# Performance work log

Measured on AMD Instinct MI355X. Metric: run time of the kernel, lower is better.

The kernel has to match this reference:

```python
import jax, jax.numpy as jnp
from jax import lax
import numpy as np

N_STEPS = 6  # fixed-grid dopri5 steps over t in [0,1] (stands in for adaptive solve at rtol=atol=1e-3)
EPS = 1e-5


def group_norm(x, w, b, groups=32):
    B, C, H, W = x.shape
    xr = x.reshape(B, groups, -1)
    m = xr.mean(-1, keepdims=True)
    v = xr.var(-1, keepdims=True)
    xn = ((xr - m) * lax.rsqrt(v + EPS)).reshape(B, C, H, W)
    return xn * w[None, :, None, None] + b[None, :, None, None]


def conv2d(x, w, b, stride, pad):
    y = lax.conv_general_dilated(x, w, (stride, stride), [(pad, pad), (pad, pad)],
                                 dimension_numbers=('NCHW', 'OIHW', 'NCHW'))
    return y + b[None, :, None, None]


def make_odefunc(oa_w, oa_b, occ1_w, occ1_b, ob_w, ob_b, occ2_w, occ2_b, oc_w, oc_b):
    def f(t, x):
        B, _, H, W = x.shape
        tt = jnp.full((B, 1, H, W), t, x.dtype)
        h = jax.nn.relu(group_norm(x, oa_w, oa_b))
        h = conv2d(jnp.concatenate([tt, h], axis=1), occ1_w, occ1_b, 1, 1)
        h = jax.nn.relu(group_norm(h, ob_w, ob_b))
        h = conv2d(jnp.concatenate([tt, h], axis=1), occ2_w, occ2_b, 1, 1)
        return group_norm(h, oc_w, oc_b)
    return f


def dopri5_fixed(f, y0, t0=0.0, t1=1.0, n=N_STEPS):
    h = (t1 - t0) / n
    def step(y, i):
        t = t0 + i * h
        k1 = f(t, y)
        k2 = f(t + h * (1/5),  y + h * (1/5) * k1)
        k3 = f(t + h * (3/10), y + h * ((3/40) * k1 + (9/40) * k2))
        k4 = f(t + h * (4/5),  y + h * ((44/45) * k1 + (-56/15) * k2 + (32/9) * k3))
        k5 = f(t + h * (8/9),  y + h * ((19372/6561) * k1 + (-25360/2187) * k2 + (64448/6561) * k3 + (-212/729) * k4))
        k6 = f(t + h,          y + h * ((9017/3168) * k1 + (-355/33) * k2 + (46732/5247) * k3 + (49/176) * k4 + (-5103/18656) * k5))
        y1 = y + h * ((35/384) * k1 + (500/1113) * k3 + (125/192) * k4 + (-2187/6784) * k5 + (11/84) * k6)
        return y1, None
    y, _ = lax.scan(step, y0, jnp.arange(n, dtype=jnp.float32))
    return y


def setup_inputs() -> dict:
    key = jax.random.key(0)
    ks = jax.random.split(key, 8)
    d = {}
    d['x'] = jax.random.normal(ks[0], (256, 3, 32, 32), jnp.float32)
    d['c1_w'] = jax.random.normal(ks[1], (64, 3, 3, 3), jnp.float32) * 0.1
    d['c1_b'] = jnp.zeros((64,), jnp.float32)
    d['g1_w'] = jnp.ones((64,), jnp.float32); d['g1_b'] = jnp.zeros((64,), jnp.float32)
    d['c2_w'] = jax.random.normal(ks[2], (64, 64, 4, 4), jnp.float32) * 0.05
    d['c2_b'] = jnp.zeros((64,), jnp.float32)
    d['g2_w'] = jnp.ones((64,), jnp.float32); d['g2_b'] = jnp.zeros((64,), jnp.float32)
    d['c3_w'] = jax.random.normal(ks[3], (64, 64, 4, 4), jnp.float32) * 0.05
    d['c3_b'] = jnp.zeros((64,), jnp.float32)
    d['oa_w'] = jnp.ones((64,), jnp.float32); d['oa_b'] = jnp.zeros((64,), jnp.float32)
    d['occ1_w'] = jax.random.normal(ks[4], (64, 65, 3, 3), jnp.float32) * 0.05
    d['occ1_b'] = jnp.zeros((64,), jnp.float32)
    d['ob_w'] = jnp.ones((64,), jnp.float32); d['ob_b'] = jnp.zeros((64,), jnp.float32)
    d['occ2_w'] = jax.random.normal(ks[5], (64, 65, 3, 3), jnp.float32) * 0.05
    d['occ2_b'] = jnp.zeros((64,), jnp.float32)
    d['oc_w'] = jnp.ones((64,), jnp.float32); d['oc_b'] = jnp.zeros((64,), jnp.float32)
    d['g3_w'] = jnp.ones((64,), jnp.float32); d['g3_b'] = jnp.zeros((64,), jnp.float32)
    d['lin_w'] = jax.random.normal(ks[6], (10, 64), jnp.float32) * 0.1
    d['lin_b'] = jnp.zeros((10,), jnp.float32)
    return d


def reference(x, c1_w, c1_b, g1_w, g1_b, c2_w, c2_b, g2_w, g2_b, c3_w, c3_b,
              oa_w, oa_b, occ1_w, occ1_b, ob_w, ob_b, occ2_w, occ2_b, oc_w, oc_b,
              g3_w, g3_b, lin_w, lin_b):
    h = jax.nn.relu(group_norm(conv2d(x, c1_w, c1_b, 1, 0), g1_w, g1_b))   # [B,64,30,30]
    h = jax.nn.relu(group_norm(conv2d(h, c2_w, c2_b, 2, 1), g2_w, g2_b))   # [B,64,15,15]
    h = conv2d(h, c3_w, c3_b, 2, 1)                                        # [B,64,7,7]
    f = make_odefunc(oa_w, oa_b, occ1_w, occ1_b, ob_w, ob_b, occ2_w, occ2_b, oc_w, oc_b)
    h = dopri5_fixed(f, h)                                                 # ODE solve t:0->1
    h = jax.nn.relu(group_norm(h, g3_w, g3_b))
    h = h.mean(axis=(2, 3))                                                # adaptive avg pool (1,1) + flatten
    return h @ lin_w.T + lin_b                                             # [B,10]
```

## Files before the change

kernel.cpp:

```cpp
#include <hip/hip_runtime.h>
#include <hip/hip_bf16.h>

#define B 256
#define NELEM 3136
#define TOTAL (B*NELEM)

typedef __attribute__((ext_vector_type(8))) short bf16x8;
typedef __attribute__((ext_vector_type(4))) float f32x4;

#define MFMA16(a,b,c) __builtin_amdgcn_mfma_f32_16x16x32_bf16((a),(b),(c),0,0,0)

__device__ __forceinline__ unsigned short f2bf(float f) {
    unsigned u = __float_as_uint(f);
    unsigned r = (u + 0x7fffu + ((u >> 16) & 1u)) >> 16;
    return (unsigned short)r;
}
__device__ __forceinline__ unsigned int f2bf2(float lo, float hi) {
    return (unsigned int)f2bf(lo) | ((unsigned int)f2bf(hi) << 16);
}

__device__ const int d_sigma[64] = {
    6,12,13,19,0,20,1,7,2,8,3,9,4,10,5,11,
    18,24,25,31,26,32,27,33,14,34,15,21,16,22,17,23,
    30,36,37,43,38,44,39,45,40,46,41,47,28,48,29,35,
    42,42,42,42,42,42,42,42,42,42,42,42,42,42,42,42
};

__global__ __launch_bounds__(256) void prep_afrag_kernel(
    const float* __restrict__ w1, const float* __restrict__ w2,
    short* __restrict__ af1, short* __restrict__ af2)
{
    const int e = blockIdx.x * 256 + threadIdx.x;
    const float* W = blockIdx.y ? w2 : w1;
    short* dst = blockIdx.y ? af2 : af1;
    const int j = e & 7;
    const int lane = (e >> 3) & 63;
    const int kt = (e >> 9) % 18;
    const int mt = (e >> 9) / 18;
    const int m = mt*16 + (lane & 15);
    const int k = kt*32 + ((lane >> 4) & 3)*8 + j;
    const int tap = k >> 6;
    const int ic  = k & 63;
    dst[e] = (short)f2bf(W[m*585 + (ic + 1)*9 + tap]);
}

__global__ __launch_bounds__(256) void prep_stab_kernel(
    const float* __restrict__ w1, const float* __restrict__ w2,
    float* __restrict__ stab1, float* __restrict__ stab2)
{
    const int id = blockIdx.x * 256 + threadIdx.x;
    if (id >= 3136) return;
    const float* W = blockIdx.y ? w2 : w1;
    float* dst = blockIdx.y ? stab2 : stab1;
    const int oc = id / 49, p = id % 49;
    const int py = p / 7, px = p % 7;
    float s = 0.f;
    #pragma unroll
    for (int ky = 0; ky < 3; ++ky) {
        int iy = py - 1 + ky;
        if (iy < 0 || iy > 6) continue;
        #pragma unroll
        for (int kx = 0; kx < 3; ++kx) {
            int ix = px - 1 + kx;
            if (ix < 0 || ix > 6) continue;
            s += W[oc*585 + ky*3 + kx];
        }
    }
    dst[id] = s;
}

__global__ __launch_bounds__(256) void prep_c1frag_kernel(
    const float* __restrict__ w1, short* __restrict__ afc1)
{
    const int e = blockIdx.x * 256 + threadIdx.x;
    const int j = e & 7, lane = (e >> 3) & 63, mtq = e >> 9;
    const int m = mtq*16 + (lane & 15);
    const int k = ((lane >> 4) & 3)*8 + j;
    float v = (k < 27) ? w1[m*27 + k] : 0.f;
    afc1[e] = (short)f2bf(v);
}

__global__ __launch_bounds__(256) void prep_c23frag_kernel(
    const float* __restrict__ w2, const float* __restrict__ w3,
    short* __restrict__ afc2, short* __restrict__ afc3)
{
    const int e = blockIdx.x * 256 + threadIdx.x;
    const float* W = blockIdx.y ? w3 : w2;
    short* dst = blockIdx.y ? afc3 : afc2;
    const int j = e & 7, lane = (e >> 3) & 63, kt = (e >> 9) & 31, mtq = e >> 14;
    const int m = mtq*16 + (lane & 15);
    const int k = kt*32 + ((lane >> 4) & 3)*8 + j;
    const int tap = k >> 6, ic = k & 63;
    dst[e] = (short)f2bf(W[m*1024 + ic*16 + tap]);
}

__global__ __launch_bounds__(512, 1) void conv1_fused(
    const float* __restrict__ x, const short* __restrict__ afc1,
    const float* __restrict__ bias,
    const float* __restrict__ g1w, const float* __restrict__ g1b,
    short* __restrict__ h1pad)
{
    __shared__ float xs[3072];
    __shared__ float gnred[128], gnq[128];
    __shared__ float s_mean[32], s_rstd[32];

    const int t = threadIdx.x, b = blockIdx.x;
    const int w = t >> 6, l = t & 63, lhi = (l >> 4) & 3, llo = l & 15;
    const int mt = w & 3, sub = w >> 2;
    const int oc0 = mt*16 + lhi*4;

    for (int i = t; i < 3072; i += 512) xs[i] = x[b*3072 + i];

    bf16x8 afr = *(const bf16x8*)(afc1 + ((size_t)(mt*64 + l))*8);

    int boff[8]; bool bval[8];
    #pragma unroll
    for (int j = 0; j < 8; ++j) {
        int k = lhi*8 + j;
        bval[j] = (k < 27);
        int kk = bval[j] ? k : 0;
        int c = kk / 9, tap = kk % 9;
        boff[j] = c*1024 + (tap/3)*32 + (tap%3);
    }
    f32x4 bia = *(const f32x4*)&bias[oc0];
    __syncthreads();

    f32x4 acc[29];
    float s[4] = {0,0,0,0}, q[4] = {0,0,0,0};
    #pragma unroll
    for (int i = 0; i < 29; ++i) {
        const int nt = sub*29 + i;
        f32x4 a = {0.f,0.f,0.f,0.f};
        if (nt < 57) {
            const int p = nt*16 + llo;
            const int pc = p < 900 ? p : 899;
            const int base = (pc/30)*32 + (pc%30);
            union { bf16x8 v; unsigned u[4]; } bb;
            #pragma unroll
            for (int jj = 0; jj < 4; ++jj) {
                float e0 = bval[2*jj]   ? xs[boff[2*jj]   + base] : 0.f;
                float e1 = bval[2*jj+1] ? xs[boff[2*jj+1] + base] : 0.f;
                bb.u[jj] = f2bf2(e0, e1);
            }
            a = MFMA16(afr, bb.v, a);
            #pragma unroll
            for (int r = 0; r < 4; ++r) {
                a[r] += bia[r];
                if (p < 900) { s[r] += a[r]; q[r] += a[r]*a[r]; }
            }
        }
        acc[i] = a;
// ... 161 lines not shown
    const float b0 = g2b[oc0], b1v_ = g2b[oc0+1], b2v_ = g2b[oc0+2], b3v_ = g2b[oc0+3];
    char* hb2 = (char*)h2pad + (size_t)b*36992;

    #pragma unroll
    for (int i = 0; i < 8; ++i) {
        const int nt = half*8 + i;
        if (nt > 14) continue;
        const int n = nt*16 + llo;
        if (n >= 225) continue;
        const int pidx = (n/15 + 1)*17 + (n%15 + 1);
        float v0 = fmaxf((acc[i][0]-m0)*rs0*w0  + b0,   0.f);
        float v1 = fmaxf((acc[i][1]-m0)*rs0*w1v + b1v_, 0.f);
        float v2 = fmaxf((acc[i][2]-m1)*rs1*w2v + b2v_, 0.f);
        float v3 = fmaxf((acc[i][3]-m1)*rs1*w3v + b3v_, 0.f);
        uint2 pk; pk.x = f2bf2(v0, v1); pk.y = f2bf2(v2, v3);
        *(uint2*)(hb2 + (oc0>>3)*4624 + pidx*16 + ((oc0&7)<<1)) = pk;
    }
    if (t < 512) {
        const int bp = t >> 3, c8 = t & 7;
        int pidx;
        if (bp < 17) pidx = bp;
        else if (bp < 34) pidx = 16*17 + (bp - 17);
        else if (bp < 49) pidx = (bp - 34 + 1)*17;
        else pidx = (bp - 49 + 1)*17 + 16;
        uint4 z; z.x = z.y = z.z = z.w = 0u;
        *(uint4*)(hb2 + c8*4624 + pidx*16) = z;
    }
}

__global__ __launch_bounds__(512, 1) void conv3_mfma(
    const short* __restrict__ h2pad, const short* __restrict__ afc3,
    const float* __restrict__ bias, float* __restrict__ y)
{
    __shared__ __align__(16) char sin[36992];
    const int t = threadIdx.x, b = blockIdx.x;
    const int w = t >> 6, l = t & 63, lhi = (l >> 4) & 3, llo = l & 15;
    const int mt = w >> 1, half = w & 1;
    const int oc0 = mt*16 + lhi*4;

    {
        const uint4* src = (const uint4*)((const char*)h2pad + (size_t)b*36992);
        uint4* dst = (uint4*)sin;
        for (int i = t; i < 2312; i += 512) dst[i] = src[i];
    }
    bf16x8 aw[32];
    #pragma unroll
    for (int kt = 0; kt < 32; ++kt)
        aw[kt] = *(const bf16x8*)(afc3 + ((size_t)((mt*32 + kt)*64 + l))*8);
    f32x4 bia = *(const f32x4*)&bias[oc0];
    __syncthreads();

    f32x4 acc[2];
    acc[0] = (f32x4){0.f,0.f,0.f,0.f};
    acc[1] = (f32x4){0.f,0.f,0.f,0.f};
    #pragma unroll
    for (int i = 0; i < 2; ++i) {
        const int nt = half*2 + i;
        const int n = nt*16 + llo;
        const int p = n < 49 ? n : 48;
        const int oy = p/7, ox = p%7;
        #pragma unroll
        for (int kt = 0; kt < 32; ++kt) {
            const int tap = kt >> 1;
            const int ky = tap >> 2, kx = tap & 3;
            const int pidx = (oy*2 + ky)*17 + (ox*2 + kx);
            const int c8 = (kt & 1)*4 + lhi;
            bf16x8 bb = *(const bf16x8*)(sin + c8*4624 + pidx*16);
            acc[i] = MFMA16(aw[kt], bb, acc[i]);
        }
    }
    #pragma unroll
    for (int i = 0; i < 2; ++i) {
        const int n = (half*2 + i)*16 + llo;
        if (n < 49) {
            #pragma unroll
            for (int r = 0; r < 4; ++r)
                y[(size_t)b*NELEM + (oc0 + r)*49 + n] = acc[i][r] + bia[r];
        }
    }
}

#define SGRP 104
#define KSTR 3328
#define ODE_LDS 115456
__global__ __launch_bounds__(512, 1) void ode_head(
    const float* __restrict__ yin,
    const short* __restrict__ af1, const short* __restrict__ af2,
    const float* __restrict__ stab1, const float* __restrict__ stab2,
    const float* __restrict__ b1v, const float* __restrict__ b2v,
    const float* __restrict__ oaw, const float* __restrict__ oab,
    const float* __restrict__ obw, const float* __restrict__ obb,
    const float* __restrict__ ocw, const float* __restrict__ ocb,
    const float* __restrict__ g3w, const float* __restrict__ g3b,
    const float* __restrict__ linw, const float* __restrict__ linb,
    float* __restrict__ out)
{
    extern __shared__ char smem[];
    float* y_l    = (float*)smem;
    float* kbuf   = (float*)(smem + 13312);
    char*  act0   = smem + 93184;
    char*  act1   = smem + 103552;
    float* gnred  = (float*)(smem + 113920);
    float* soaw   = (float*)(smem + 114432);
    float* soab   = (float*)(smem + 114688);
    float* s_mean = (float*)(smem + 114944);
    float* s_rstd = (float*)(smem + 115072);
    float* s_cm   = (float*)(smem + 115200);

    const int t = threadIdx.x, b = blockIdx.x;
    const int w = t >> 6, l = t & 63, lhi = (l >> 4) & 3, llo = l & 15;
    const int mt = w >> 1;
    const int ntA = (w & 1)*2, ntB = ntA + 1;
    const int nA = ntA*16 + llo, nB = ntB*16 + llo;
    const bool vA = nA < 49, vB = nB < 49;
    const int pxA = d_sigma[nA], pxB = d_sigma[nB];
    const int paA = (pxA/7 + 1)*9 + (pxA%7 + 1);
    const int paB = (pxB/7 + 1)*9 + (pxB%7 + 1);
    const int oc0 = mt*16 + lhi*4;
    const int g16 = t >> 4, sub = t & 15;

    for (int u = t; u < 3136; u += 512) {
        const int g = u / 98, e = u - g*98;
        y_l[g*SGRP + e] = yin[(size_t)b*NELEM + u];
    }
    for (int i = t; i < 5184; i += 512) ((unsigned*)act0)[i] = 0u;
    if (t < 64) { soaw[t] = oaw[t]; soab[t] = oab[t]; }

    float stabA1[4], stabB1[4], stabA2[4], stabB2[4];
    #pragma unroll
    for (int r = 0; r < 4; ++r) {
        stabA1[r] = stab1[(oc0 + r)*49 + pxA];
        stabB1[r] = stab1[(oc0 + r)*49 + pxB];
        stabA2[r] = stab2[(oc0 + r)*49 + pxA];
        stabB2[r] = stab2[(oc0 + r)*49 + pxB];
    }
    const f32x4 bia1 = *(const f32x4*)&b1v[oc0];
    const f32x4 bia2 = *(const f32x4*)&b2v[oc0];
    const f32x4 gwB = *(const f32x4*)&obw[oc0];
    const f32x4 gbB = *(const f32x4*)&obb[oc0];
    const f32x4 gwC = *(const f32x4*)&ocw[oc0];
    const f32x4 gbC = *(const f32x4*)&ocb[oc0];
    __syncthreads();

    const float hf  = (float)(1.0/6.0);
    const float C10 = (float)((1.0/6.0)*(1.0/5.0));
    const float C20 = (float)((1.0/6.0)*(3.0/40.0)),  C21 = (float)((1.0/6.0)*(9.0/40.0));
    const float C30 = (float)((1.0/6.0)*(44.0/45.0)), C31 = (float)((1.0/6.0)*(-56.0/15.0)), C32 = (float)((1.0/6.0)*(32.0/9.0));
    const float C40 = (float)((1.0/6.0)*(19372.0/6561.0)), C41 = (float)((1.0/6.0)*(-25360.0/2187.0)),
                C42 = (float)((1.0/6.0)*(64448.0/6561.0)), C43 = (float)((1.0/6.0)*(-212.0/729.0));
    const float C50 = (float)((1.0/6.0)*(9017.0/3168.0)), C51 = (float)((1.0/6.0)*(-355.0/33.0)),
                C52 = (float)((1.0/6.0)*(46732.0/5247.0)), C53 = (float)((1.0/6.0)*(49.0/176.0)),
                C54 = (float)((1.0/6.0)*(-5103.0/18656.0));
    const float B0 = (float)((1.0/6.0)*(35.0/384.0)), B2c = (float)((1.0/6.0)*(500.0/1113.0)),
                B3c = (float)((1.0/6.0)*(125.0/192.0)), B4c = (float)((1.0/6.0)*(-2187.0/6784.0)),
                B5c = (float)((1.0/6.0)*(11.0/84.0));

    for (int step = 0; step < 6; ++step) {
        const float t0 = (float)step * hf;
        for (int stage = 0; stage < 6; ++stage) {
            float cA=0.f, cB=0.f, cC=0.f, cD=0.f, cE=0.f, tf=0.f;
            if (stage == 1)      { cA=C10; tf = 0.2f; }
            else if (stage == 2) { cA=C20; cB=C21; tf = 0.3f; }
            else if (stage == 3) { cA=C30; cB=C31; cC=C32; tf = 0.8f; }
            else if (stage == 4) { cA=C40; cB=C41; cC=C42; cD=C43; tf = (float)(8.0/9.0); }
            else if (stage == 5) { cA=C50; cB=C51; cC=C52; cD=C53; cE=C54; tf = 1.f; }
            const float tval = t0 + hf*tf;

            {
                const float* Yg = y_l + g16*SGRP;
                const float* Kg = kbuf + g16*SGRP;
                const int e0 = 4*sub;
                const int n1 = (sub < 8) ? 4 : ((sub == 8) ? 2 : 0);
                const int e1 = 64 + 4*sub;

                f32x4 va, vb = {0.f,0.f,0.f,0.f};
                {
                    f32x4 xv = *(const f32x4*)(Yg + e0);
                    if (stage > 0) xv += cA * *(const f32x4*)(Kg + 0*KSTR + e0);
                    if (stage > 1) xv += cB * *(const f32x4*)(Kg + 1*KSTR + e0);
                    if (stage > 2) xv += cC * *(const f32x4*)(Kg + 2*KSTR + e0);
                    if (stage > 3) xv += cD * *(const f32x4*)(Kg + 3*KSTR + e0);
                    if (stage > 4) xv += cE * *(const f32x4*)(Kg + 4*KSTR + e0);
                    va = xv;
                }
                if (n1 == 4) {
                    f32x4 xv = *(const f32x4*)(Yg + e1);
                    if (stage > 0) xv += cA * *(const f32x4*)(Kg + 0*KSTR + e1);
                    if (stage > 1) xv += cB * *(const f32x4*)(Kg + 1*KSTR + e1);
                    if (stage > 2) xv += cC * *(const f32x4*)(Kg + 2*KSTR + e1);
                    if (stage > 3) xv += cD * *(const f32x4*)(Kg + 3*KSTR + e1);
                    if (stage > 4) xv += cE * *(const f32x4*)(Kg + 4*KSTR + e1);
                    vb = xv;
                } else if (n1 == 2) {
                    float x0 = Yg[96], x1 = Yg[97];
                    if (stage > 0) { x0 = fmaf(cA, Kg[0*KSTR+96], x0); x1 = fmaf(cA, Kg[0*KSTR+97], x1); }
                    if (stage > 1) { x0 = fmaf(cB, Kg[1*KSTR+96], x0); x1 = fmaf(cB, Kg[1*KSTR+97], x1); }
                    if (stage > 2) { x0 = fmaf(cC, Kg[2*KSTR+96], x0); x1 = fmaf(cC, Kg[2*KSTR+97], x1); }
                    if (stage > 3) { x0 = fmaf(cD, Kg[3*KSTR+96], x0); x1 = fmaf(cD, Kg[3*KSTR+97], x1); }
                    if (stage > 4) { x0 = fmaf(cE, Kg[4*KSTR+96], x0); x1 = fmaf(cE, Kg[4*KSTR+97], x1); }
                    vb[0] = x0; vb[1] = x1;
                }

                float s = va[0]+va[1]+va[2]+va[3];
                float q = va[0]*va[0]+va[1]*va[1]+va[2]*va[2]+va[3]*va[3];
                if (n1 >= 2) { s += vb[0]+vb[1]; q += vb[0]*vb[0]+vb[1]*vb[1]; }
                if (n1 == 4) { s += vb[2]+vb[3]; q += vb[2]*vb[2]+vb[3]*vb[3]; }
                s += __shfl_xor(s, 1); q += __shfl_xor(q, 1);
                s += __shfl_xor(s, 2); q += __shfl_xor(q, 2);
                s += __shfl_xor(s, 4); q += __shfl_xor(q, 4);
                s += __shfl_xor(s, 8); q += __shfl_xor(q, 8);
                const float m = s * (1.f/98.f);
                const float rs = rsqrtf(q * (1.f/98.f) - m*m + 1e-5f);
                const float w0 = soaw[2*g16], w1s = soaw[2*g16+1];
                const float bb0 = soab[2*g16], bb1 = soab[2*g16+1];

                #pragma unroll
                for (int j2 = 0; j2 < 4; ++j2) {
                    const int e = e0 + j2;
                    const int odd = e >= 49 ? 1 : 0;
                    const int ch = 2*g16 + odd;
                    const int p = e - 49*odd;
                    float nv = fmaxf((va[j2] - m)*rs*(odd ? w1s : w0) + (odd ? bb1 : bb0), 0.f);
                    const int pa = (p/7 + 1)*9 + (p%7) + 1;
                    *(unsigned short*)(act0 + (ch>>3)*1296 + pa*16 + ((ch&7)<<1)) = f2bf(nv);
                }
                for (int j2 = 0; j2 < n1; ++j2) {
                    const int e = e1 + j2;
                    const int odd = e >= 49 ? 1 : 0;
                    const int ch = 2*g16 + odd;
                    const int p = e - 49*odd;
                    float nv = fmaxf((vb[j2] - m)*rs*(odd ? w1s : w0) + (odd ? bb1 : bb0), 0.f);
                    const int pa = (p/7 + 1)*9 + (p%7) + 1;
                    *(unsigned short*)(act0 + (ch>>3)*1296 + pa*16 + ((ch&7)<<1)) = f2bf(nv);
                }
            }
            __syncthreads();

            float v0[4], v1[4];
            {
                bf16x8 aw[18];
                #pragma unroll
                for (int kt = 0; kt < 18; ++kt)
                    aw[kt] = *(const bf16x8*)(af1 + ((size_t)(mt*18 + kt)*64 + l)*8);
                f32x4 acc0 = {0.f,0.f,0.f,0.f}, acc1 = {0.f,0.f,0.f,0.f};
                #pragma unroll
                for (int kt = 0; kt < 18; ++kt) {
                    const int tap = kt >> 1;
                    const int dB = ((tap/3 - 1)*9 + (tap%3 - 1))*16;
                    const int cb = ((kt & 1)*4 + lhi)*1296;
                    bf16x8 bb0 = *(const bf16x8*)(act0 + cb + paA*16 + dB);
                    bf16x8 bb1 = *(const bf16x8*)(act0 + cb + paB*16 + dB);
                    acc0 = MFMA16(aw[kt], bb0, acc0);
                    acc1 = MFMA16(aw[kt], bb1, acc1);
                }
                #pragma unroll
                for (int r = 0; r < 4; ++r) {
                    v0[r] = acc0[r] + bia1[r] + tval * stabA1[r];
                    v1[r] = acc1[r] + bia1[r] + tval * stabB1[r];
                }
            }
            {
                float s0=0.f,q0=0.f,s1=0.f,q1=0.f;
                if (vA) { s0 += v0[0]+v0[1]; q0 += v0[0]*v0[0]+v0[1]*v0[1];
                          s1 += v0[2]+v0[3]; q1 += v0[2]*v0[2]+v0[3]*v0[3]; }
                if (vB) { s0 += v1[0]+v1[1]; q0 += v1[0]*v1[0]+v1[1]*v1[1];
                          s1 += v1[2]+v1[3]; q1 += v1[2]*v1[2]+v1[3]*v1[3]; }
                #pragma unroll
                for (int off = 1; off < 16; off <<= 1) {
                    s0 += __shfl_xor(s0, off); q0 += __shfl_xor(q0, off);
                    s1 += __shfl_xor(s1, off); q1 += __shfl_xor(q1, off);
                }
                if (llo == 0) {
                    float* gp = gnred + w*16 + lhi*4;
                    gp[0]=s0; gp[1]=q0; gp[2]=s1; gp[3]=q1;
                }
            }
            __syncthreads();
            {
                const int gb = mt*32 + lhi*4;
                const float sg0 = gnred[gb]   + gnred[gb+16];
                const float qg0 = gnred[gb+1] + gnred[gb+17];
                const float sg1 = gnred[gb+2] + gnred[gb+18];
                const float qg1 = gnred[gb+3] + gnred[gb+19];
                const float m0 = sg0*(1.f/98.f);
                const float r0 = rsqrtf(qg0*(1.f/98.f) - m0*m0 + 1e-5f);
                const float m1 = sg1*(1.f/98.f);
                const float r1 = rsqrtf(qg1*(1.f/98.f) - m1*m1 + 1e-5f);
                v0[0] = fmaxf((v0[0]-m0)*r0*gwB[0]+gbB[0], 0.f);
                v0[1] = fmaxf((v0[1]-m0)*r0*gwB[1]+gbB[1], 0.f);
                v0[2] = fmaxf((v0[2]-m1)*r1*gwB[2]+gbB[2], 0.f);
                v0[3] = fmaxf((v0[3]-m1)*r1*gwB[3]+gbB[3], 0.f);
                v1[0] = fmaxf((v1[0]-m0)*r0*gwB[0]+gbB[0], 0.f);
                v1[1] = fmaxf((v1[1]-m0)*r0*gwB[1]+gbB[1], 0.f);
                v1[2] = fmaxf((v1[2]-m1)*r1*gwB[2]+gbB[2], 0.f);
                v1[3] = fmaxf((v1[3]-m1)*r1*gwB[3]+gbB[3], 0.f);
                if (vA) {
                    uint2 pk; pk.x = f2bf2(v0[0], v0[1]); pk.y = f2bf2(v0[2], v0[3]);
                    *(uint2*)(act1 + (oc0>>3)*1296 + paA*16 + ((oc0&7)<<1)) = pk;
                }
                if (vB) {
                    uint2 pk; pk.x = f2bf2(v1[0], v1[1]); pk.y = f2bf2(v1[2], v1[3]);
                    *(uint2*)(act1 + (oc0>>3)*1296 + paB*16 + ((oc0&7)<<1)) = pk;
                }
            }
            __syncthreads();

            {
                bf16x8 aw[18];
                #pragma unroll
                for (int kt = 0; kt < 18; ++kt)
                    aw[kt] = *(const bf16x8*)(af2 + ((size_t)(mt*18 + kt)*64 + l)*8);
                f32x4 acc0 = {0.f,0.f,0.f,0.f}, acc1 = {0.f,0.f,0.f,0.f};
                #pragma unroll
                for (int kt = 0; kt < 18; ++kt) {
                    const int tap = kt >> 1;
                    const int dB = ((tap/3 - 1)*9 + (tap%3 - 1))*16;
                    const int cb = ((kt & 1)*4 + lhi)*1296;
                    bf16x8 bb0 = *(const bf16x8*)(act1 + cb + paA*16 + dB);
                    bf16x8 bb1 = *(const bf16x8*)(act1 + cb + paB*16 + dB);
                    acc0 = MFMA16(aw[kt], bb0, acc0);
                    acc1 = MFMA16(aw[kt], bb1, acc1);
                }
                #pragma unroll
                for (int r = 0; r < 4; ++r) {
                    v0[r] = acc0[r] + bia2[r] + tval * stabA2[r];
                    v1[r] = acc1[r] + bia2[r] + tval * stabB2[r];
                }
            }
            {
                float s0=0.f,q0=0.f,s1=0.f,q1=0.f;
                if (vA) { s0 += v0[0]+v0[1]; q0 += v0[0]*v0[0]+v0[1]*v0[1];
                          s1 += v0[2]+v0[3]; q1 += v0[2]*v0[2]+v0[3]*v0[3]; }
                if (vB) { s0 += v1[0]+v1[1]; q0 += v1[0]*v1[0]+v1[1]*v1[1];
                          s1 += v1[2]+v1[3]; q1 += v1[2]*v1[2]+v1[3]*v1[3]; }
                #pragma unroll
                for (int off = 1; off < 16; off <<= 1) {
                    s0 += __shfl_xor(s0, off); q0 += __shfl_xor(q0, off);
                    s1 += __shfl_xor(s1, off); q1 += __shfl_xor(q1, off);
                }
                if (llo == 0) {
                    float* gp = gnred + w*16 + lhi*4;
                    gp[0]=s0; gp[1]=q0; gp[2]=s1; gp[3]=q1;
                }
            }
            __syncthreads();
            {
                const int gb = mt*32 + lhi*4;
                const float sg0 = gnred[gb]   + gnred[gb+16];
                const float qg0 = gnred[gb+1] + gnred[gb+17];
                const float sg1 = gnred[gb+2] + gnred[gb+18];
                const float qg1 = gnred[gb+3] + gnred[gb+19];
                const float m0 = sg0*(1.f/98.f);
                const float r0 = rsqrtf(qg0*(1.f/98.f) - m0*m0 + 1e-5f);
                const float m1 = sg1*(1.f/98.f);
                const float r1 = rsqrtf(qg1*(1.f/98.f) - m1*m1 + 1e-5f);
                float* kd = kbuf + stage*KSTR;
                const int gA = oc0 >> 1;
                if (vA) {
                    kd[gA*SGRP + pxA]            = (v0[0]-m0)*r0*gwC[0]+gbC[0];
                    kd[gA*SGRP + 49 + pxA]       = (v0[1]-m0)*r0*gwC[1]+gbC[1];
                    kd[(gA+1)*SGRP + pxA]        = (v0[2]-m1)*r1*gwC[2]+gbC[2];
                    kd[(gA+1)*SGRP + 49 + pxA]   = (v0[3]-m1)*r1*gwC[3]+gbC[3];
                }
                if (vB) {
                    kd[gA*SGRP + pxB]            = (v1[0]-m0)*r0*gwC[0]+gbC[0];
                    kd[gA*SGRP + 49 + pxB]       = (v1[1]-m0)*r0*gwC[1]+gbC[1];
                    kd[(gA+1)*SGRP + pxB]        = (v1[2]-m1)*r1*gwC[2]+gbC[2];
                    kd[(gA+1)*SGRP + 49 + pxB]   = (v1[3]-m1)*r1*gwC[3]+gbC[3];
                }
            }
            __syncthreads();

            if (stage == 5) {
                float* Yg = y_l + g16*SGRP;
                const float* Kg = kbuf + g16*SGRP;
                const int e0 = 4*sub;
                {
                    f32x4 v = *(const f32x4*)(Yg + e0);
                    v += B0  * *(const f32x4*)(Kg + 0*KSTR + e0);
                    v += B2c * *(const f32x4*)(Kg + 2*KSTR + e0);
                    v += B3c * *(const f32x4*)(Kg + 3*KSTR + e0);
                    v += B4c * *(const f32x4*)(Kg + 4*KSTR + e0);
                    v += B5c * *(const f32x4*)(Kg + 5*KSTR + e0);
                    *(f32x4*)(Yg + e0) = v;
                }
                if (sub < 8) {
                    const int e1 = 64 + 4*sub;
                    f32x4 v = *(const f32x4*)(Yg + e1);
                    v += B0  * *(const f32x4*)(Kg + 0*KSTR + e1);
                    v += B2c * *(const f32x4*)(Kg + 2*KSTR + e1);
                    v += B3c * *(const f32x4*)(Kg + 3*KSTR + e1);
                    v += B4c * *(const f32x4*)(Kg + 4*KSTR + e1);
                    v += B5c * *(const f32x4*)(Kg + 5*KSTR + e1);
                    *(f32x4*)(Yg + e1) = v;
                } else if (sub == 8) {
                    #pragma unroll
                    for (int j2 = 0; j2 < 2; ++j2) {
                        const int e = 96 + j2;
                        float v = Yg[e];
                        v = fmaf(B0,  Kg[0*KSTR+e], v);
                        v = fmaf(B2c, Kg[2*KSTR+e], v);
                        v = fmaf(B3c, Kg[3*KSTR+e], v);
                        v = fmaf(B4c, Kg[4*KSTR+e], v);
                        v = fmaf(B5c, Kg[5*KSTR+e], v);
                        Yg[e] = v;
                    }
                }
                __syncthreads();
            }
        }
    }

    {
        float s = 0.f, q = 0.f;
        const float* Yg = y_l + g16*SGRP;
        for (int e = sub; e < 98; e += 16) {
            float v = Yg[e];
            s += v; q += v*v;
        }
        s += __shfl_xor(s,1); q += __shfl_xor(q,1);
        s += __shfl_xor(s,2); q += __shfl_xor(q,2);
        s += __shfl_xor(s,4); q += __shfl_xor(q,4);
        s += __shfl_xor(s,8); q += __shfl_xor(q,8);
        if (sub == 0) {
            float m = s * (1.f/98.f);
            float var = q * (1.f/98.f) - m*m;
            s_mean[g16] = m; s_rstd[g16] = rsqrtf(var + 1e-5f);
        }
    }
    __syncthreads();
    if (t < 64) {
        const int ch = t, g = ch >> 1;
        const float m = s_mean[g], r = s_rstd[g];
        const float ww = g3w[ch], bb = g3b[ch];
        const float* Yc = y_l + g*SGRP + (ch & 1)*49;
        float sum = 0.f;
        for (int p = 0; p < 49; ++p) {
            float v = (Yc[p] - m)*r*ww + bb;
            sum += fmaxf(v, 0.f);
        }
        s_cm[ch] = sum * (1.f/49.f);
    }
    __syncthreads();
    if (t < 10) {
        float a = linb[t];
        for (int c = 0; c < 64; ++c) a = fmaf(s_cm[c], linw[t*64 + c], a);
        out[b*10 + t] = a;
    }
}

extern "C" void kernel_launch(void* const* d_in, const int* in_sizes, int n_in,
                              void* d_out, int out_size, void* d_ws, size_t ws_size,
                              hipStream_t stream)
{
    const float* x      = (const float*)d_in[0];
    const float* c1_w   = (const float*)d_in[1];
    const float* c1_b   = (const float*)d_in[2];
    const float* g1_w   = (const float*)d_in[3];
    const float* g1_b   = (const float*)d_in[4];
    const float* c2_w   = (const float*)d_in[5];
    const float* c2_b   = (const float*)d_in[6];
    const float* g2_w   = (const float*)d_in[7];
    const float* g2_b   = (const float*)d_in[8];
    const float* c3_w   = (const float*)d_in[9];
    const float* c3_b   = (const float*)d_in[10];
    const float* oa_w   = (const float*)d_in[11];
    const float* oa_b   = (const float*)d_in[12];
    const float* occ1_w = (const float*)d_in[13];
    const float* occ1_b = (const float*)d_in[14];
    const float* ob_w   = (const float*)d_in[15];
    const float* ob_b   = (const float*)d_in[16];
    const float* occ2_w = (const float*)d_in[17];
    const float* occ2_b = (const float*)d_in[18];
    const float* oc_w   = (const float*)d_in[19];
    const float* oc_b   = (const float*)d_in[20];
    const float* g3_w   = (const float*)d_in[21];
    const float* g3_b   = (const float*)d_in[22];
    const float* lin_w  = (const float*)d_in[23];
    const float* lin_b  = (const float*)d_in[24];
    float* out = (float*)d_out;

    float* ws = (float*)d_ws;
    size_t off = 0;
    float* y     = ws + off; off += 802816;
    float* stab1 = ws + off; off += 3136;
    float* stab2 = ws + off; off += 3136;
    short* af1   = (short*)(ws + off); off += 18432;
    short* af2   = (short*)(ws + off); off += 18432;
    short* afc1  = (short*)(ws + off); off += 1024;
    short* afc2  = (short*)(ws + off); off += 32768;
    short* afc3  = (short*)(ws + off); off += 32768;
    short* h1pad = (short*)(ws + off); off += 8396800;
    short* h2pad = (short*)(ws + off); off += 2367488;

    prep_afrag_kernel<<<dim3(144, 2), 256, 0, stream>>>(occ1_w, occ2_w, af1, af2);
    prep_stab_kernel<<<dim3(13, 2), 256, 0, stream>>>(occ1_w, occ2_w, stab1, stab2);
    prep_c1frag_kernel<<<8, 256, 0, stream>>>(c1_w, afc1);
    prep_c23frag_kernel<<<dim3(256, 2), 256, 0, stream>>>(c2_w, c3_w, afc2, afc3);

    conv1_fused<<<B, 512, 0, stream>>>(x, afc1, c1_b, g1_w, g1_b, h1pad);
    conv2_fused<<<B, 512, CONV2_LDS, stream>>>(h1pad, afc2, c2_b, g2_w, g2_b, h2pad);
    conv3_mfma<<<B, 512, 0, stream>>>(h2pad, afc3, c3_b, y);

    ode_head<<<B, 512, ODE_LDS, stream>>>(y, af1, af2, stab1, stab2,
        occ1_b, occ2_b, oa_w, oa_b, ob_w, ob_b, oc_w, oc_b,
        g3_w, g3_b, lin_w, lin_b, out);
}
```

Baseline: 251.7 us.

## Switch ODE convs to 32x32 MFMA with register-resident weights and wave specialization

Replaces the 16x16x32 MFMA ODE convolutions with 32x32x16 MFMA. The time channel is folded into two extra K channels in the activation buffer, which removes the precomputed t*stab correction. Weight fragments for both convs are preloaded once into registers, with waves 0-1 running conv1 and waves 2-3 running conv2. Group-norm reductions now happen within a wave via shuffles instead of through LDS, removing one barrier per conv. The cost is that only 2 of 8 waves do MFMA work in each phase, and the kernel carries heavy register pressure from holding 37 bf16x8 fragments plus 32 accumulators.

Measured after the change: 453.6 us. 1.8x slower.

```diff
diff --git a/kernel.cpp b/kernel.cpp
--- a/kernel.cpp
+++ b/kernel.cpp
@@ -5,10 +5,12 @@
 #define NELEM 3136
 #define TOTAL (B*NELEM)
 
-typedef __attribute__((ext_vector_type(8))) short bf16x8;
-typedef __attribute__((ext_vector_type(4))) float f32x4;
+typedef __attribute__((ext_vector_type(8)))  short bf16x8;
+typedef __attribute__((ext_vector_type(4)))  float f32x4;
+typedef __attribute__((ext_vector_type(16))) float f32x16;
 
 #define MFMA16(a,b,c) __builtin_amdgcn_mfma_f32_16x16x32_bf16((a),(b),(c),0,0,0)
+#define MFMA32(a,b,c) __builtin_amdgcn_mfma_f32_32x32x16_bf16((a),(b),(c),0,0,0)
 
 __device__ __forceinline__ unsigned short f2bf(float f) {
     unsigned u = __float_as_uint(f);
@@ -18,55 +20,40 @@
 __device__ __forceinline__ unsigned int f2bf2(float lo, float hi) {
     return (unsigned int)f2bf(lo) | ((unsigned int)f2bf(hi) << 16);
 }
-
-__device__ const int d_sigma[64] = {
-    6,12,13,19,0,20,1,7,2,8,3,9,4,10,5,11,
-    18,24,25,31,26,32,27,33,14,34,15,21,16,22,17,23,
-    30,36,37,43,38,44,39,45,40,46,41,47,28,48,29,35,
-    42,42,42,42,42,42,42,42,42,42,42,42,42,42,42,42
+__device__ __forceinline__ unsigned int cvtpk(float lo, float hi) {
+    unsigned int r;
+    asm("v_cvt_pk_bf16_f32 %0, %1, %2" : "=v"(r) : "v"(lo), "v"(hi));
+    return r;
+}
+
+__device__ const int d_sig32[64] = {
+     6,13, 0, 1, 2, 3, 4, 5,  12,19,20, 7, 8, 9,10,11,
+    18,25,26,27,14,15,16,17,  24,31,32,33,34,21,22,23,
+    30,37,38,39,40,41,28,29,  36,43,44,45,46,47,48,35,
+    42,13, 0, 1, 2, 3, 4, 5,   6,13, 0, 1, 2, 3, 4, 5
 };
 
-__global__ __launch_bounds__(256) void prep_afrag_kernel(
+__global__ __launch_bounds__(256) void prep_af32(
     const float* __restrict__ w1, const float* __restrict__ w2,
-    short* __restrict__ af1, short* __restrict__ af2)
+    short* __restrict__ af1x, short* __restrict__ af2x)
 {
     const int e = blockIdx.x * 256 + threadIdx.x;
+    if (e >= 37888) return;
     const float* W = blockIdx.y ? w2 : w1;
-    short* dst = blockIdx.y ? af2 : af1;
-    const int j = e & 7;
-    const int lane = (e >> 3) & 63;
-    const int kt = (e >> 9) % 18;
-    const int mt = (e >> 9) / 18;
-    const int m = mt*16 + (lane & 15);
-    const int k = kt*32 + ((lane >> 4) & 3)*8 + j;
-    const int tap = k >> 6;
-    const int ic  = k & 63;
-    dst[e] = (short)f2bf(W[m*585 + (ic + 1)*9 + tap]);
-}
-
-__global__ __launch_bounds__(256) void prep_stab_kernel(
-    const float* __restrict__ w1, const float* __restrict__ w2,
-    float* __restrict__ stab1, float* __restrict__ stab2)
-{
-    const int id = blockIdx.x * 256 + threadIdx.x;
-    if (id >= 3136) return;
-    const float* W = blockIdx.y ? w2 : w1;
-    float* dst = blockIdx.y ? stab2 : stab1;
-    const int oc = id / 49, p = id % 49;
-    const int py = p / 7, px = p % 7;
-    float s = 0.f;
-    #pragma unroll
-    for (int ky = 0; ky < 3; ++ky) {
-        int iy = py - 1 + ky;
-        if (iy < 0 || iy > 6) continue;
-        #pragma unroll
-        for (int kx = 0; kx < 3; ++kx) {
-            int ix = px - 1 + kx;
-            if (ix < 0 || ix > 6) continue;
-            s += W[oc*585 + ky*3 + kx];
-        }
-    }
-    dst[id] = s;
+    short* dst = blockIdx.y ? af2x : af1x;
+    const int j = e & 7, lane = (e >> 3) & 63, r = e >> 9;
+    const int kt = r % 37, mh = r / 37;
+    const int m = mh*32 + (lane & 31);
+    const int kk = (lane >> 5)*8 + j;
+    float val;
+    if (kt < 36) {
+        const int tap = kt >> 2;
+        const int ic  = (kt & 3)*16 + kk;
+        val = W[m*585 + (ic + 1)*9 + tap];
+    } else {
+        val = (kk < 9) ? W[m*585 + kk] : 0.f;
+    }
+    dst[e] = (short)f2bf(val);
 }
 
 __global__ __launch_bounds__(256) void prep_c1frag_kernel(
@@ -394,11 +381,19 @@
 
 #define SGRP 104
 #define KSTR 3328
-#define ODE_LDS 115456
-__global__ __launch_bounds__(512, 1) void ode_head(
+#define ACT_C8 1296
+#define ODE_LDS 121408
+#define P_B1 0
+#define P_B2 64
+#define P_GWB 128
+#define P_GBB 192
+#define P_GWC 256
+#define P_GBC 320
+#define P_OAW 384
+#define P_OAB 448
+__global__ __launch_bounds__(512, 2) void ode_head(
     const float* __restrict__ yin,
-    const short* __restrict__ af1, const short* __restrict__ af2,
-    const float* __restrict__ stab1, const float* __restrict__ stab2,
+    const short* __restrict__ af1x, const short* __restrict__ af2x,
     const float* __restrict__ b1v, const float* __restrict__ b2v,
     const float* __restrict__ oaw, const float* __restrict__ oab,
     const float* __restrict__ obw, const float* __restrict__ obb,
@@ -408,50 +403,41 @@
     float* __restrict__ out)
 {
     extern __shared__ char smem[];
-    float* y_l    = (float*)smem;
-    float* kbuf   = (float*)(smem + 13312);
-    char*  act0   = smem + 93184;
-    char*  act1   = smem + 103552;
-    float* gnred  = (float*)(smem + 113920);
-    float* soaw   = (float*)(smem + 114432);
-    float* soab   = (float*)(smem + 114688);
-    float* s_mean = (float*)(smem + 114944);
-    float* s_rstd = (float*)(smem + 115072);
-    float* s_cm   = (float*)(smem + 115200);
+    float* y_l  = (float*)smem;
+    float* kbuf = (float*)(smem + 13312);
+    char*  act0 = smem + 93184;
+    char*  act1 = smem + 106144;
+    float* prm  = (float*)(smem + 119104);
+    float* s_cm = (float*)(smem + 121152);
 
     const int t = threadIdx.x, b = blockIdx.x;
-    const int w = t >> 6, l = t & 63, lhi = (l >> 4) & 3, llo = l & 15;
-    const int mt = w >> 1;
-    const int ntA = (w & 1)*2, ntB = ntA + 1;
-    const int nA = ntA*16 + llo, nB = ntB*16 + llo;
-    const bool vA = nA < 49, vB = nB < 49;
-    const int pxA = d_sigma[nA], pxB = d_sigma[nB];
-    const int paA = (pxA/7 + 1)*9 + (pxA%7 + 1);
-    const int paB = (pxB/7 + 1)*9 + (pxB%7 + 1);
-    const int oc0 = mt*16 + lhi*4;
+    const int w = t >> 6, l = t & 63;
     const int g16 = t >> 4, sub = t & 15;
+
+    const int hi_ = l >> 5;
+    const int ln  = l & 31;
+    const int px0 = d_sig32[ln], px1 = d_sig32[32 + ln];
+    const bool val1 = (32 + ln) <= 48;
+    const int pa0 = (px0/7 + 1)*9 + (px0%7 + 1);
+    const int pa1 = (px1/7 + 1)*9 + (px1%7 + 1);
+    const int mh = w & 1;
 
     for (int u = t; u < 3136; u += 512) {
         const int g = u / 98, e = u - g*98;
         y_l[g*SGRP + e] = yin[(size_t)b*NELEM + u];
     }
-    for (int i = t; i < 5184; i += 512) ((unsigned*)act0)[i] = 0u;
-    if (t < 64) { soaw[t] = oaw[t]; soab[t] = oab[t]; }
-
-    float stabA1[4], stabB1[4], stabA2[4], stabB2[4];
-    #pragma unroll
-    for (int r = 0; r < 4; ++r) {
-        stabA1[r] = stab1[(oc0 + r)*49 + pxA];
-        stabB1[r] = stab1[(oc0 + r)*49 + pxB];
-        stabA2[r] = stab2[(oc0 + r)*49 + pxA];
-        stabB2[r] = stab2[(oc0 + r)*49 + pxB];
-    }
-    const f32x4 bia1 = *(const f32x4*)&b1v[oc0];
-    const f32x4 bia2 = *(const f32x4*)&b2v[oc0];
-    const f32x4 gwB = *(const f32x4*)&obw[oc0];
-    const f32x4 gbB = *(const f32x4*)&obb[oc0];
-    const f32x4 gwC = *(const f32x4*)&ocw[oc0];
-    const f32x4 gbC = *(const f32x4*)&ocb[oc0];
+    for (int i = t; i < 6480; i += 512) ((unsigned*)act0)[i] = 0u;
+    if (t < 64) {
+        prm[P_B1  + t] = b1v[t]; prm[P_B2  + t] = b2v[t];
+        prm[P_GWB + t] = obw[t]; prm[P_GBB + t] = obb[t];
+        prm[P_GWC + t] = ocw[t]; prm[P_GBC + t] = ocb[t];
+        prm[P_OAW + t] = oaw[t]; prm[P_OAB + t] = oab[t];
+    }
+    const short* aft = (w < 2) ? af1x : af2x;
+    bf16x8 afr[37];
+    #pragma unroll
+    for (int kt = 0; kt < 37; ++kt)
+        afr[kt] = *(const bf16x8*)(aft + ((size_t)(mh*37 + kt)*64 + l)*8);
     __syncthreads();
 
     const float hf  = (float)(1.0/6.0);
@@ -523,8 +509,8 @@
                 s += __shfl_xor(s, 8); q += __shfl_xor(q, 8);
                 const float m = s * (1.f/98.f);
                 const float rs = rsqrtf(q * (1.f/98.f) - m*m + 1e-5f);
-                const float w0 = soaw[2*g16], w1s = soaw[2*g16+1];
-                const float bb0 = soab[2*g16], bb1 = soab[2*g16+1];
+                const float w0 = prm[P_OAW + 2*g16], w1c = prm[P_OAW + 2*g16 + 1];
+                const float c0 = prm[P_OAB + 2*g16], c1c = prm[P_OAB + 2*g16 + 1];
 
                 #pragma unroll
                 for (int j2 = 0; j2 < 4; ++j2) {
@@ -532,153 +518,184 @@
                     const int odd = e >= 49 ? 1 : 0;
                     const int ch = 2*g16 + odd;
                     const int p = e - 49*odd;
-                    float nv = fmaxf((va[j2] - m)*rs*(odd ? w1s : w0) + (odd ? bb1 : bb0), 0.f);
+                    float nv = fmaxf((va[j2] - m)*rs*(odd ? w1c : w0) + (odd ? c1c : c0), 0.f);
                     const int pa = (p/7 + 1)*9 + (p%7) + 1;
-                    *(unsigned short*)(act0 + (ch>>3)*1296 + pa*16 + ((ch&7)<<1)) = f2bf(nv);
+                    *(unsigned short*)(act0 + (ch>>3)*ACT_C8 + pa*16 + ((ch&7)<<1)) = f2bf(nv);
                 }
                 for (int j2 = 0; j2 < n1; ++j2) {
                     const int e = e1 + j2;
                     const int odd = e >= 49 ? 1 : 0;
                     const int ch = 2*g16 + odd;
                     const int p = e - 49*odd;
-                    float nv = fmaxf((vb[j2] - m)*rs*(odd ? w1s : w0) + (odd ? bb1 : bb0), 0.f);
+                    float nv = fmaxf((vb[j2] - m)*rs*(odd ? w1c : w0) + (odd ? c1c : c0), 0.f);
                     const int pa = (p/7 + 1)*9 + (p%7) + 1;
-                    *(unsigned short*)(act0 + (ch>>3)*1296 + pa*16 + ((ch&7)<<1)) = f2bf(nv);
-                }
+                    *(unsigned short*)(act0 + (ch>>3)*ACT_C8 + pa*16 + ((ch&7)<<1)) = f2bf(nv);
+                }
+            }
+            if (w == 7 && l < 49) {
+                const int py = l / 7, pxx = l % 7;
+                const int pa = (py + 1)*9 + (pxx + 1);
+                const unsigned tb = (unsigned)f2bf(tval);
+                unsigned h[8];
+                #pragma unroll
+                for (int tap = 0; tap < 8; ++tap) {
+                    const int dy = tap/3 - 1, dx = tap%3 - 1;
+                    const bool ok = ((unsigned)(py+dy) < 7u) && ((unsigned)(pxx+dx) < 7u);
+                    h[tap] = ok ? tb : 0u;
+                }
+                uint4 blkA;
+                blkA.x = h[0] | (h[1]<<16); blkA.y = h[2] | (h[3]<<16);
+                blkA.z = h[4] | (h[5]<<16); blkA.w = h[6] | (h[7]<<16);
+                const bool ok8 = (py+1) < 7 && (pxx+1) < 7;
+                uint4 blkB; blkB.x = ok8 ? tb : 0u; blkB.y = 0u; blkB.z = 0u; blkB.w = 0u;
+                *(uint4*)(act0 + 8*ACT_C8 + pa*16) = blkA;
+                *(uint4*)(act0 + 9*ACT_C8 + pa*16) = blkB;
+                *(uint4*)(act1 + 8*ACT_C8 + pa*16) = blkA;
+                *(uint4*)(act1 + 9*ACT_C8 + pa*16) = blkB;
             }
             __syncthreads();
 
-            float v0[4], v1[4];
-            {
-                bf16x8 aw[18];
-                #pragma unroll
-                for (int kt = 0; kt < 18; ++kt)
-                    aw[kt] = *(const bf16x8*)(af1 + ((size_t)(mt*18 + kt)*64 + l)*8);
-                f32x4 acc0 = {0.f,0.f,0.f,0.f}, acc1 = {0.f,0.f,0.f,0.f};
-                #pragma unroll
-                for (int kt = 0; kt < 18; ++kt) {
-                    const int tap = kt >> 1;
-                    const int dB = ((tap/3 - 1)*9 + (tap%3 - 1))*16;
-                    const int cb = ((kt & 1)*4 + lhi)*1296;
-                    bf16x8 bb0 = *(const bf16x8*)(act0 + cb + paA*16 + dB);
-                    bf16x8 bb1 = *(const bf16x8*)(act0 + cb + paB*16 + dB);
-                    acc0 = MFMA16(aw[kt], bb0, acc0);
-                    acc1 = MFMA16(aw[kt], bb1, acc1);
-                }
-                #pragma unroll
-                for (int r = 0; r < 4; ++r) {
-                    v0[r] = acc0[r] + bia1[r] + tval * stabA1[r];
-                    v1[r] = acc1[r] + bia1[r] + tval * stabB1[r];
-                }
-            }
-            {
-                float s0=0.f,q0=0.f,s1=0.f,q1=0.f;
-                if (vA) { s0 += v0[0]+v0[1]; q0 += v0[0]*v0[0]+v0[1]*v0[1];
-                          s1 += v0[2]+v0[3]; q1 += v0[2]*v0[2]+v0[3]*v0[3]; }
-                if (vB) { s0 += v1[0]+v1[1]; q0 += v1[0]*v1[0]+v1[1]*v1[1];
-                          s1 += v1[2]+v1[3]; q1 += v1[2]*v1[2]+v1[3]*v1[3]; }
-                #pragma unroll
-                for (int off = 1; off < 16; off <<= 1) {
-                    s0 += __shfl_xor(s0, off); q0 += __shfl_xor(q0, off);
-                    s1 += __shfl_xor(s1, off); q1 += __shfl_xor(q1, off);
-                }
-                if (llo == 0) {
-                    float* gp = gnred + w*16 + lhi*4;
-                    gp[0]=s0; gp[1]=q0; gp[2]=s1; gp[3]=q1;
+            if (w < 2) {
+                f32x16 a0, a1;
+                #pragma unroll
+                for (int i = 0; i < 16; ++i) { a0[i] = 0.f; a1[i] = 0.f; }
+                #pragma unroll
+                for (int kt = 0; kt < 37; ++kt) {
+                    int cb, dB;
+                    if (kt < 36) {
+                        const int tap = kt >> 2;
+                        dB = ((tap/3 - 1)*9 + (tap%3 - 1))*16;
+                        cb = ((kt & 3)*2 + hi_)*ACT_C8;
+                    } else { dB = 0; cb = (8 + hi_)*ACT_C8; }
+                    bf16x8 b0 = *(const bf16x8*)(act0 + cb + pa0*16 + dB);
+                    bf16x8 b1 = *(const bf16x8*)(act0 + cb + pa1*16 + dB);
+                    a0 = MFMA32(afr[kt], b0, a0);
+                    a1 = MFMA32(afr[kt], b1, a1);
+                }
+                #pragma unroll
+                for (int qd = 0; qd < 4; ++qd) {
+                    f32x4 bia = *(const f32x4*)&prm[P_B1 + mh*32 + qd*8 + 4*hi_];
+                    #pragma unroll
+                    for (int j = 0; j < 4; ++j) { a0[qd*4+j] += bia[j]; a1[qd*4+j] += bia[j]; }
+                }
+                float gm[8], gr[8];
+                {
+                    float gs[8], gq[8];
+                    #pragma unroll
+                    for (int qd = 0; qd < 4; ++qd)
+                        #pragma unroll
+                        for (int u = 0; u < 2; ++u) {
+                            const int i0 = qd*4 + 2*u;
+                            float s = a0[i0] + a0[i0+1];
+                            float qq = a0[i0]*a0[i0] + a0[i0+1]*a0[i0+1];
+                            if (val1) { s += a1[i0] + a1[i0+1]; qq += a1[i0]*a1[i0] + a1[i0+1]*a1[i0+1]; }
+                            gs[qd*2+u] = s; gq[qd*2+u] = qq;
+                        }
+                    #pragma unroll
+                    for (int off = 1; off < 32; off <<= 1)
+                        #pragma unroll
+                        for (int i = 0; i < 8; ++i) {
+                            gs[i] += __shfl_xor(gs[i], off);
+                            gq[i] += __shfl_xor(gq[i], off);
+                        }
+                    #pragma unroll
+                    for (int i = 0; i < 8; ++i) {
+                        const float m = gs[i]*(1.f/98.f);
+                        gm[i] = m; gr[i] = rsqrtf(gq[i]*(1.f/98.f) - m*m + 1e-5f);
+                    }
+                }
+                #pragma unroll
+                for (int qd = 0; qd < 4; ++qd) {
+                    f32x4 gw = *(const f32x4*)&prm[P_GWB + mh*32 + qd*8 + 4*hi_];
+                    f32x4 gc = *(const f32x4*)&prm[P_GBB + mh*32 + qd*8 + 4*hi_];
+                    const int c8 = mh*4 + qd;
+                    float x0[4], x1[4];
+                    #pragma unroll
+                    for (int u = 0; u < 2; ++u) {
+                        const float m = gm[qd*2+u], r = gr[qd*2+u];
+                        #pragma unroll
+                        for (int j = 0; j < 2; ++j) {
+                            const int i = qd*4 + 2*u + j;
+                            x0[2*u+j] = fmaxf((a0[i]-m)*r*gw[2*u+j] + gc[2*u+j], 0.f);
+                            x1[2*u+j] = fmaxf((a1[i]-m)*r*gw[2*u+j] + gc[2*u+j], 0.f);
+                        }
+                    }
+                    uint2 p0; p0.x = cvtpk(x0[0], x0[1]); p0.y = cvtpk(x0[2], x0[3]);
+                    *(uint2*)(act1 + c8*ACT_C8 + pa0*16 + hi_*8) = p0;
+                    if (val1) {
+                        uint2 p1; p1.x = cvtpk(x1[0], x1[1]); p1.y = cvtpk(x1[2], x1[3]);
+                        *(uint2*)(act1 + c8*ACT_C8 + pa1*16 + hi_*8) = p1;
+                    }
                 }
             }
             __syncthreads();
-            {
-                const int gb = mt*32 + lhi*4;
-                const float sg0 = gnred[gb]   + gnred[gb+16];
-                const float qg0 = gnred[gb+1] + gnred[gb+17];
-                const float sg1 = gnred[gb+2] + gnred[gb+18];
-                const float qg1 = gnred[gb+3] + gnred[gb+19];
-                const float m0 = sg0*(1.f/98.f);
-                const float r0 = rsqrtf(qg0*(1.f/98.f) - m0*m0 + 1e-5f);
-                const float m1 = sg1*(1.f/98.f);
-                const float r1 = rsqrtf(qg1*(1.f/98.f) - m1*m1 + 1e-5f);
-                v0[0] = fmaxf((v0[0]-m0)*r0*gwB[0]+gbB[0], 0.f);
-                v0[1] = fmaxf((v0[1]-m0)*r0*gwB[1]+gbB[1], 0.f);
-                v0[2] = fmaxf((v0[2]-m1)*r1*gwB[2]+gbB[2], 0.f);
-                v0[3] = fmaxf((v0[3]-m1)*r1*gwB[3]+gbB[3], 0.f);
-                v1[0] = fmaxf((v1[0]-m0)*r0*gwB[0]+gbB[0], 0.f);
-                v1[1] = fmaxf((v1[1]-m0)*r0*gwB[1]+gbB[1], 0.f);
-                v1[2] = fmaxf((v1[2]-m1)*r1*gwB[2]+gbB[2], 0.f);
-                v1[3] = fmaxf((v1[3]-m1)*r1*gwB[3]+gbB[3], 0.f);
-                if (vA) {
-                    uint2 pk; pk.x = f2bf2(v0[0], v0[1]); pk.y = f2bf2(v0[2], v0[3]);
-                    *(uint2*)(act1 + (oc0>>3)*1296 + paA*16 + ((oc0&7)<<1)) = pk;
-                }
-                if (vB) {
-                    uint2 pk; pk.x = f2bf2(v1[0], v1[1]); pk.y = f2bf2(v1[2], v1[3]);
-                    *(uint2*)(act1 + (oc0>>3)*1296 + paB*16 + ((oc0&7)<<1)) = pk;
-                }
-            }
-            __syncthreads();
-
-            {
-                bf16x8 aw[18];
-                #pragma unroll
-                for (int kt = 0; kt < 18; ++kt)
-                    aw[kt] = *(const bf16x8*)(af2 + ((size_t)(mt*18 + kt)*64 + l)*8);
-                f32x4 acc0 = {0.f,0.f,0.f,0.f}, acc1 = {0.f,0.f,0.f,0.f};
-                #pragma unroll
-                for (int kt = 0; kt < 18; ++kt) {
-                    const int tap = kt >> 1;
-                    const int dB = ((tap/3 - 1)*9 + (tap%3 - 1))*16;
-                    const int cb = ((kt & 1)*4 + lhi)*1296;
-                    bf16x8 bb0 = *(const bf16x8*)(act1 + cb + paA*16 + dB);
-                    bf16x8 bb1 = *(const bf16x8*)(act1 + cb + paB*16 + dB);
-                    acc0 = MFMA16(aw[kt], bb0, acc0);
-                    acc1 = MFMA16(aw[kt], bb1, acc1);
-                }
-                #pragma unroll
-                for (int r = 0; r < 4; ++r) {
-                    v0[r] = acc0[r] + bia2[r] + tval * stabA2[r];
-                    v1[r] = acc1[r] + bia2[r] + tval * stabB2[r];
-                }
-            }
-            {
-                float s0=0.f,q0=0.f,s1=0.f,q1=0.f;
-                if (vA) { s0 += v0[0]+v0[1]; q0 += v0[0]*v0[0]+v0[1]*v0[1];
-                          s1 += v0[2]+v0[3]; q1 += v0[2]*v0[2]+v0[3]*v0[3]; }
-                if (vB) { s0 += v1[0]+v1[1]; q0 += v1[0]*v1[0]+v1[1]*v1[1];
-                          s1 += v1[2]+v1[3]; q1 += v1[2]*v1[2]+v1[3]*v1[3]; }
-                #pragma unroll
-                for (int off = 1; off < 16; off <<= 1) {
-                    s0 += __shfl_xor(s0, off); q0 += __shfl_xor(q0, off);
-                    s1 += __shfl_xor(s1, off); q1 += __shfl_xor(q1, off);
-                }
-                if (llo == 0) {
-                    float* gp = gnred + w*16 + lhi*4;
-                    gp[0]=s0; gp[1]=q0; gp[2]=s1; gp[3]=q1;
-                }
-            }
-            __syncthreads();
-            {
-                const int gb = mt*32 + lhi*4;
-                const float sg0 = gnred[gb]   + gnred[gb+16];
-                const float qg0 = gnred[gb+1] + gnred[gb+17];
-                const float sg1 = gnred[gb+2] + gnred[gb+18];
-                const float qg1 = gnred[gb+3] + gnred[gb+19];
-                const float m0 = sg0*(1.f/98.f);
-                const float r0 = rsqrtf(qg0*(1.f/98.f) - m0*m0 + 1e-5f);
-                const float m1 = sg1*(1.f/98.f);
-                const float r1 = rsqrtf(qg1*(1.f/98.f) - m1*m1 + 1e-5f);
+
+            if (w >= 2 && w < 4) {
+                f32x16 a0, a1;
+                #pragma unroll
+                for (int i = 0; i < 16; ++i) { a0[i] = 0.f; a1[i] = 0.f; }
+                #pragma unroll
+                for (int kt = 0; kt < 37; ++kt) {
+                    int cb, dB;
+                    if (kt < 36) {
+                        const int tap = kt >> 2;
+                        dB = ((tap/3 - 1)*9 + (tap%3 - 1))*16;
+                        cb = ((kt & 3)*2 + hi_)*ACT_C8;
+                    } else { dB = 0; cb = (8 + hi_)*ACT_C8; }
+                    bf16x8 b0 = *(const bf16x8*)(act1 + cb + pa0*16 + dB);
+                    bf16x8 b1 = *(const bf16x8*)(act1 + cb + pa1*16 + dB);
+                    a0 = MFMA32(afr[kt], b0, a0);
+                    a1 = MFMA32(afr[kt], b1, a1);
+                }
+                #pragma unroll
+                for (int qd = 0; qd < 4; ++qd) {
+                    f32x4 bia = *(const f32x4*)&prm[P_B2 + mh*32 + qd*8 + 4*hi_];
+                    #pragma unroll
+                    for (int j = 0; j < 4; ++j) { a0[qd*4+j] += bia[j]; a1[qd*4+j] += bia[j]; }
+                }
+                float gm[8], gr[8];
+                {
+                    float gs[8], gq[8];
+                    #pragma unroll
+                    for (int qd = 0; qd < 4; ++qd)
+                        #pragma unroll
+                        for (int u = 0; u < 2; ++u) {
+                            const int i0 = qd*4 + 2*u;
+                            float s = a0[i0] + a0[i0+1];
+                            float qq = a0[i0]*a0[i0] + a0[i0+1]*a0[i0+1];
+                            if (val1) { s += a1[i0] + a1[i0+1]; qq += a1[i0]*a1[i0] + a1[i0+1]*a1[i0+1]; }
+                            gs[qd*2+u] = s; gq[qd*2+u] = qq;
+                        }
+                    #pragma unroll
+                    for (int off = 1; off < 32; off <<= 1)
+                        #pragma unroll
+                        for (int i = 0; i < 8; ++i) {
+                            gs[i] += __shfl_xor(gs[i], off);
+                            gq[i] += __shfl_xor(gq[i], off);
+                        }
+                    #pragma unroll
+                    for (int i = 0; i < 8; ++i) {
+                        const float m = gs[i]*(1.f/98.f);
+                        gm[i] = m; gr[i] = rsqrtf(gq[i]*(1.f/98.f) - m*m + 1e-5f);
+                    }
+                }
                 float* kd = kbuf + stage*KSTR;
-                const int gA = oc0 >> 1;
-                if (vA) {
-                    kd[gA*SGRP + pxA]            = (v0[0]-m0)*r0*gwC[0]+gbC[0];
-                    kd[gA*SGRP + 49 + pxA]       = (v0[1]-m0)*r0*gwC[1]+gbC[1];
-                    kd[(gA+1)*SGRP + pxA]        = (v0[2]-m1)*r1*gwC[2]+gbC[2];
-                    kd[(gA+1)*SGRP + 49 + pxA]   = (v0[3]-m1)*r1*gwC[3]+gbC[3];
-                }
-                if (vB) {
-                    kd[gA*SGRP + pxB]            = (v1[0]-m0)*r0*gwC[0]+gbC[0];
-                    kd[gA*SGRP + 49 + pxB]       = (v1[1]-m0)*r0*gwC[1]+gbC[1];
-                    kd[(gA+1)*SGRP + pxB]        = (v1[2]-m1)*r1*gwC[2]+gbC[2];
-                    kd[(gA+1)*SGRP + 49 + pxB]   = (v1[3]-m1)*r1*gwC[3]+gbC[3];
+                #pragma unroll
+                for (int qd = 0; qd < 4; ++qd) {
+                    f32x4 gw = *(const f32x4*)&prm[P_GWC + mh*32 + qd*8 + 4*hi_];
+                    f32x4 gc = *(const f32x4*)&prm[P_GBC + mh*32 + qd*8 + 4*hi_];
+                    #pragma unroll
+                    for (int u = 0; u < 2; ++u) {
+                        const float m = gm[qd*2+u], r = gr[qd*2+u];
+                        const int ch0 = mh*32 + qd*8 + 4*hi_ + 2*u;
+                        const int gg = ch0 >> 1;
+                        kd[gg*SGRP + px0]      = (a0[qd*4+2*u]   - m)*r*gw[2*u]   + gc[2*u];
+                        kd[gg*SGRP + 49 + px0] = (a0[qd*4+2*u+1] - m)*r*gw[2*u+1] + gc[2*u+1];
+                        if (val1) {
+                            kd[gg*SGRP + px1]      = (a1[qd*4+2*u]   - m)*r*gw[2*u]   + gc[2*u];
+                            kd[gg*SGRP + 49 + px1] = (a1[qd*4+2*u+1] - m)*r*gw[2*u+1] + gc[2*u+1];
+                        }
+                    }
                 }
             }
             __syncthreads();
@@ -723,6 +740,7 @@
         }
     }
 
+    float* hstat = kbuf;
     {
         float s = 0.f, q = 0.f;
         const float* Yg = y_l + g16*SGRP;
@@ -737,13 +755,13 @@
         if (sub == 0) {
             float m = s * (1.f/98.f);
             float var = q * (1.f/98.f) - m*m;
-            s_mean[g16] = m; s_rstd[g16] = rsqrtf(var + 1e-5f);
+            hstat[g16] = m; hstat[32 + g16] = rsqrtf(var + 1e-5f);
         }
     }
     __syncthreads();
     if (t < 64) {
         const int ch = t, g = ch >> 1;
-        const float m = s_mean[g], r = s_rstd[g];
+        const float m = hstat[g], r = hstat[32 + g];
         const float ww = g3w[ch], bb = g3b[ch];
         const float* Yc = y_l + g*SGRP + (ch & 1)*49;
         float sum = 0.f;
@@ -795,18 +813,15 @@
     float* ws = (float*)d_ws;
     size_t off = 0;
     float* y     = ws + off; off += 802816;
-    float* stab1 = ws + off; off += 3136;
-    float* stab2 = ws + off; off += 3136;
-    short* af1   = (short*)(ws + off); off += 18432;
-    short* af2   = (short*)(ws + off); off += 18432;
+    short* af1x  = (short*)(ws + off); off += 18944;
+    short* af2x  = (short*)(ws + off); off += 18944;
     short* afc1  = (short*)(ws + off); off += 1024;
     short* afc2  = (short*)(ws + off); off += 32768;
     short* afc3  = (short*)(ws + off); off += 32768;
     short* h1pad = (short*)(ws + off); off += 8396800;
     short* h2pad = (short*)(ws + off); off += 2367488;
 
-    prep_afrag_kernel<<<dim3(144, 2), 256, 0, stream>>>(occ1_w, occ2_w, af1, af2);
-    prep_stab_kernel<<<dim3(13, 2), 256, 0, stream>>>(occ1_w, occ2_w, stab1, stab2);
+    prep_af32<<<dim3(148, 2), 256, 0, stream>>>(occ1_w, occ2_w, af1x, af2x);
     prep_c1frag_kernel<<<8, 256, 0, stream>>>(c1_w, afc1);
     prep_c23frag_kernel<<<dim3(256, 2), 256, 0, stream>>>(c2_w, c3_w, afc2, afc3);
 
@@ -814,7 +829,7 @@
     conv2_fused<<<B, 512, CONV2_LDS, stream>>>(h1pad, afc2, c2_b, g2_w, g2_b, h2pad);
     conv3_mfma<<<B, 512, 0, stream>>>(h2pad, afc3, c3_b, y);
 
-    ode_head<<<B, 512, ODE_LDS, stream>>>(y, af1, af2, stab1, stab2,
+    ode_head<<<B, 512, ODE_LDS, stream>>>(y, af1x, af2x,
         occ1_b, occ2_b, oa_w, oa_b, ob_w, ob_b, oc_w, oc_b,
         g3_w, g3_b, lin_w, lin_b, out);
 }
```
